# Kernel tuning notes

Hardware: AMD Instinct MI355X
Metric: run time of the kernel (lower is better)

Reference implementation:

```python
import jax, jax.numpy as jnp
import numpy as np

N, E = 20000, 320000
EPS = 1e-5
NEG_SLOPE = 0.2


def gat_conv(x, src, dst, W, att_src, att_dst, bias, num_nodes):
    # W: [Fin, H*C], att_*: [H, C], bias: [H*C]
    H, C = att_src.shape
    h = (x @ W).reshape(num_nodes, H, C)            # [N,H,C]
    a_s = jnp.einsum('nhc,hc->nh', h, att_src)      # [N,H]
    a_d = jnp.einsum('nhc,hc->nh', h, att_dst)      # [N,H]
    e = jax.nn.leaky_relu(a_s[src] + a_d[dst], NEG_SLOPE)  # [E,H]
    m = jax.ops.segment_max(e, dst, num_segments=num_nodes)       # per-dst max (self-loops guarantee non-empty)
    ex = jnp.exp(e - m[dst])
    s = jax.ops.segment_sum(ex, dst, num_segments=num_nodes)
    alpha = ex / s[dst]                              # [E,H] segment softmax
    out = jax.ops.segment_sum(h[src] * alpha[:, :, None], dst, num_segments=num_nodes)  # [N,H,C]
    return out.reshape(num_nodes, H * C) + bias


def batch_norm(x, gamma, beta):
    mu = x.mean(axis=0)
    var = x.var(axis=0)  # biased, as torch BN uses for normalization
    return (x - mu) * jax.lax.rsqrt(var + EPS) * gamma + beta


def setup_inputs() -> dict:
    key = jax.random.key(0)
    ks = jax.random.split(key, 32)
    x = jax.random.normal(ks[0], (N, 512), dtype=jnp.float32)
    edge_index = jax.random.randint(ks[1], (2, E), 0, N, dtype=jnp.int32)
    d = {"x": x, "edge_index": edge_index}
    # layer configs: (Fin, C_out, H)
    cfgs = [(512, 64, 8), (512, 64, 4), (256, 64, 2), (128, 16, 1)]
    i = 2
    for li, (fin, c, h) in enumerate(cfgs, start=1):
        sc = 1.0 / np.sqrt(fin)
        d[f"W{li}"] = jax.random.normal(ks[i], (fin, h * c), dtype=jnp.float32) * sc; i += 1
        d[f"as{li}"] = jax.random.normal(ks[i], (h, c), dtype=jnp.float32) * 0.1; i += 1
        d[f"ad{li}"] = jax.random.normal(ks[i], (h, c), dtype=jnp.float32) * 0.1; i += 1
        d[f"b{li}"] = jnp.zeros((h * c,), dtype=jnp.float32)
        if li < 4:
            d[f"g{li}"] = jnp.ones((h * c,), dtype=jnp.float32)
            d[f"be{li}"] = jnp.zeros((h * c,), dtype=jnp.float32)
    return d


def reference(x, edge_index, W1, as1, ad1, b1, g1, be1, W2, as2, ad2, b2, g2, be2, W3, as3, ad3, b3, g3, be3, W4, as4, ad4, b4):
    num_nodes = x.shape[0]
    loop = jnp.arange(num_nodes, dtype=edge_index.dtype)
    src = jnp.concatenate([edge_index[0], loop])  # add_self_loops=True
    dst = jnp.concatenate([edge_index[1], loop])
    h = gat_conv(x, src, dst, W1, as1, ad1, b1, num_nodes)
    h = jax.nn.elu(batch_norm(h, g1, be1))
    h = gat_conv(h, src, dst, W2, as2, ad2, b2, num_nodes)
    h = jax.nn.elu(batch_norm(h, g2, be2))
    h = gat_conv(h, src, dst, W3, as3, ad3, b3, num_nodes)
    h = jax.nn.elu(batch_norm(h, g3, be3))
    h = gat_conv(h, src, dst, W4, as4, ad4, b4, num_nodes)
    return jax.nn.log_softmax(h, axis=1)
```

## Files before the change

kernel.cpp:

```cpp
#include <hip/hip_runtime.h>
#include <hip/hip_bf16.h>
#include <cstdint>
#include <cstddef>

#define NN 20000
#define EE 320000
#define ET (EE + NN)
#define MPAD 20096
#define SCHUNK 20

typedef __attribute__((ext_vector_type(8))) short  short8;
typedef __attribute__((ext_vector_type(4))) float  floatx4;

__device__ inline unsigned short f2bf(float f) {
    unsigned u = __float_as_uint(f);
    u += 0x7FFFu + ((u >> 16) & 1u);
    return (unsigned short)(u >> 16);
}
__device__ inline float bf2f(unsigned short b) {
    return __uint_as_float(((unsigned)b) << 16);
}
__device__ inline float bflo(unsigned u) { return __uint_as_float(u << 16); }
__device__ inline float bfhi(unsigned u) { return __uint_as_float(u & 0xFFFF0000u); }

__global__ void zero_i32(int* __restrict__ p, int n) {
    int i = blockIdx.x * blockDim.x + threadIdx.x;
    if (i < n) p[i] = 0;
}

__global__ void cvt_a_bf16(const float* __restrict__ in, unsigned short* __restrict__ out,
                           int M, int Mpad, int K) {
    long long base = ((long long)blockIdx.x * blockDim.x + threadIdx.x) * 4;
    if (base >= (long long)Mpad * K) return;
    int row = (int)(base / K);
    float4 v = make_float4(0.f, 0.f, 0.f, 0.f);
    if (row < M) v = *(const float4*)(in + base);
    ushort4 o;
    o.x = f2bf(v.x); o.y = f2bf(v.y); o.z = f2bf(v.z); o.w = f2bf(v.w);
    *(ushort4*)(out + base) = o;
}

#define W1SZ (512 * 512)
#define W2SZ (512 * 256)
#define W3SZ (256 * 128)
__global__ void cvt_w_all(const float* __restrict__ W1, unsigned short* __restrict__ Wt1,
                          const float* __restrict__ W2, unsigned short* __restrict__ Wt2,
                          const float* __restrict__ W3, unsigned short* __restrict__ Wt3) {
    int i = blockIdx.x * blockDim.x + threadIdx.x;
    const float* W; unsigned short* Wt; int K, N, idx;
    if (i < W1SZ)               { W = W1; Wt = Wt1; K = 512; N = 512; idx = i; }
    else if (i < W1SZ + W2SZ)   { W = W2; Wt = Wt2; K = 512; N = 256; idx = i - W1SZ; }
    else if (i < W1SZ + W2SZ + W3SZ) { W = W3; Wt = Wt3; K = 256; N = 128; idx = i - W1SZ - W2SZ; }
    else return;
    int k = idx / N, n = idx - k * N;
    Wt[(size_t)n * K + k] = f2bf(W[idx]);
}

__global__ void count_edges(const int* __restrict__ dst, int* __restrict__ cnt) {
    int e = blockIdx.x * blockDim.x + threadIdx.x;
    if (e >= ET) return;
    int d = (e < EE) ? dst[e] : (e - EE);
    atomicAdd(&cnt[d], 1);
}

__global__ __launch_bounds__(1024) void scan_fast(const int* __restrict__ cnt,
                                                  int* __restrict__ rowp,
                                                  int* __restrict__ wptr, int n) {
    __shared__ int sums[1024];
    const int t = threadIdx.x;
    const int base = t * SCHUNK;
    int local[SCHUNK];
    int acc = 0;
#pragma unroll
    for (int i = 0; i < SCHUNK; ++i) {
        int idx = base + i;
        int v = (idx < n) ? cnt[idx] : 0;
        local[i] = acc;
        acc += v;
    }
    sums[t] = acc;
    __syncthreads();
    for (int o = 1; o < 1024; o <<= 1) {
        int u = (t >= o) ? sums[t - o] : 0;
        __syncthreads();
        sums[t] += u;
        __syncthreads();
    }
    int excl = sums[t] - acc;
#pragma unroll
    for (int i = 0; i < SCHUNK; ++i) {
        int idx = base + i;
        if (idx < n) { int rp = excl + local[i]; rowp[idx] = rp; wptr[idx] = rp; }
    }
    if (t == 1023) rowp[n] = sums[1023];
}

__global__ void fill_edges(const int* __restrict__ src, const int* __restrict__ dst,
                           int* __restrict__ wptr, int* __restrict__ colx) {
    int e = blockIdx.x * blockDim.x + threadIdx.x;
    if (e >= ET) return;
    int s, d;
    if (e < EE) { s = src[e]; d = dst[e]; } else { s = e - EE; d = e - EE; }
    int pos = atomicAdd(&wptr[d], 1);
    colx[pos] = s;
}

__global__ __launch_bounds__(256) void gemm_bf16_fused(
        const unsigned short* __restrict__ A, const unsigned short* __restrict__ Bt,
        unsigned short* __restrict__ hN, float* __restrict__ aS, float* __restrict__ aD,
        const float* __restrict__ atts, const float* __restrict__ attd,
        int M, int N, int K) {
    __shared__ unsigned short As[128][40];
    __shared__ unsigned short Bs[128][40];
    const int t = threadIdx.x;
    const int lane = t & 63, wave = t >> 6;
    const int wm = wave >> 1, wn = wave & 1;
    const int quad = lane >> 4, mrow = lane & 15;
    const int row0 = blockIdx.y * 128, col0 = blockIdx.x * 128;
    const int srow = t >> 2, schunk = (t & 3) * 8;

    floatx4 acc[4][4];
#pragma unroll
    for (int i = 0; i < 4; ++i)
#pragma unroll
        for (int j = 0; j < 4; ++j)
#pragma unroll
            for (int r = 0; r < 4; ++r) acc[i][j][r] = 0.f;

    for (int k0 = 0; k0 < K; k0 += 32) {
        uint4 ra0 = *(const uint4*)(A  + (size_t)(row0 + srow)      * K + k0 + schunk);
        uint4 ra1 = *(const uint4*)(A  + (size_t)(row0 + srow + 64) * K + k0 + schunk);
        uint4 rb0 = *(const uint4*)(Bt + (size_t)(col0 + srow)      * K + k0 + schunk);
        uint4 rb1 = *(const uint4*)(Bt + (size_t)(col0 + srow + 64) * K + k0 + schunk);
        __syncthreads();
        *(uint4*)&As[srow][schunk]      = ra0;
        *(uint4*)&As[srow + 64][schunk] = ra1;
        *(uint4*)&Bs[srow][schunk]      = rb0;
        *(uint4*)&Bs[srow + 64][schunk] = rb1;
        __syncthreads();

        short8 af[4], bfr[4];
#pragma unroll
        for (int i = 0; i < 4; ++i)
            af[i] = *(const short8*)&As[wm * 64 + i * 16 + mrow][quad * 8];
#pragma unroll
        for (int j = 0; j < 4; ++j)
            bfr[j] = *(const short8*)&Bs[wn * 64 + j * 16 + mrow][quad * 8];
#pragma unroll
        for (int i = 0; i < 4; ++i)
#pragma unroll
            for (int j = 0; j < 4; ++j)
                acc[i][j] = __builtin_amdgcn_mfma_f32_16x16x32_bf16(af[i], bfr[j], acc[i][j], 0, 0, 0);
    }

    const int head = (col0 + wn * 64) >> 6;
    float attS[4], attD[4];
#pragma unroll
    for (int j = 0; j < 4; ++j) {
        attS[j] = atts[head * 64 + j * 16 + mrow];
        attD[j] = attd[head * 64 + j * 16 + mrow];
    }

#pragma unroll
    for (int i = 0; i < 4; ++i) {
#pragma unroll
        for (int r = 0; r < 4; ++r) {
            int row = row0 + wm * 64 + i * 16 + quad * 4 + r;
            float ps = acc[i][0][r] * attS[0] + acc[i][1][r] * attS[1]
                     + acc[i][2][r] * attS[2] + acc[i][3][r] * attS[3];
            float pd = acc[i][0][r] * attD[0] + acc[i][1][r] * attD[1]
                     + acc[i][2][r] * attD[2] + acc[i][3][r] * attD[3];
#pragma unroll
            for (int o = 1; o < 16; o <<= 1) {
                ps += __shfl_xor(ps, o);
                pd += __shfl_xor(pd, o);
            }
            if (row < M) {
                if (mrow == 0) {
                    aS[(size_t)head * M + row] = ps;
                    aD[(size_t)head * M + row] = pd;
                }
#pragma unroll
                for (int j = 0; j < 4; ++j)
                    hN[(size_t)row * N + col0 + wn * 64 + j * 16 + mrow] = f2bf(acc[i][j][r]);
            }
        }
    }
}

template <int HH>
__global__ __launch_bounds__(256) void gat_agg_head32(
        const unsigned short* __restrict__ hN,
        const float* __restrict__ aS, const float* __restrict__ aD,
        const int* __restrict__ rowp, const int* __restrict__ colx,
        const float* __restrict__ bias, float* __restrict__ out,
        float* __restrict__ part, int Nn) {
    constexpr int F = HH * 64;
    constexpr int G = 8 / HH;
    __shared__ uint2 pair[4][4][33];
    __shared__ float red[4][16][9];
    const int L = blockIdx.x;
    const int x8 = L & 7;
    const int hd = x8 / G;
    const int nodeblk = (L >> 3) * G + (x8 & (G - 1));
    const int wave = threadIdx.x >> 6, lane = threadIdx.x & 63;
    const int grp = lane >> 4;
    const int q   = lane & 15;
    const int n = nodeblk * 16 + wave * 4 + grp;
    const bool valid = (n < Nn);

    float4 o4 = make_float4(0.f, 0.f, 0.f, 0.f);

    if (valid) {
        const float* aSh = aS + (size_t)hd * Nn;
        const float adv = aD[(size_t)hd * Nn + n];
        const int b0 = rowp[n], b1 = rowp[n + 1];
        const unsigned short* hbase = hN + hd * 64;

        float m, s;
        float a0 = 0.f, a1 = 0.f, a2 = 0.f, a3 = 0.f;

        auto gather = [&](int cnt) {
            const int iters = (cnt + 3) >> 2;
            for (int it = 0; it < iters; ++it) {
                const int j = it << 2;
                uint2 x0 = pair[wave][grp][j + 0];
                uint2 x1 = pair[wave][grp][j + 1];
                uint2 x2 = pair[wave][grp][j + 2];
                uint2 x3 = pair[wave][grp][j + 3];
                uint2 v0 = *(const uint2*)(hbase + (size_t)x0.x * F + q * 4);
                uint2 v1 = *(const uint2*)(hbase + (size_t)x1.x * F + q * 4);
                uint2 v2 = *(const uint2*)(hbase + (size_t)x2.x * F + q * 4);
                uint2 v3 = *(const uint2*)(hbase + (size_t)x3.x * F + q * 4);
                float p0 = __uint_as_float(x0.y), p1 = __uint_as_float(x1.y);
                float p2 = __uint_as_float(x2.y), p3 = __uint_as_float(x3.y);
                a0 += p0 * bflo(v0.x) + p1 * bflo(v1.x) + p2 * bflo(v2.x) + p3 * bflo(v3.x);
                a1 += p0 * bfhi(v0.x) + p1 * bfhi(v1.x) + p2 * bfhi(v2.x) + p3 * bfhi(v3.x);
                a2 += p0 * bflo(v0.y) + p1 * bflo(v1.y) + p2 * bflo(v2.y) + p3 * bflo(v3.y);
                a3 += p0 * bfhi(v0.y) + p1 * bfhi(v1.y) + p2 * bfhi(v2.y) + p3 * bfhi(v3.y);
            }
        };

        {
            const int cnt = min(32, b1 - b0);
            int sn0 = 0, sn1 = 0;
            if (q < cnt)      sn0 = colx[b0 + q];
            if (q + 16 < cnt) sn1 = colx[b0 + q + 16];
            float t0 = aSh[sn0] + adv;
            float t1 = aSh[sn1] + adv;
            float e0 = (q < cnt)      ? ((t0 > 0.f) ? t0 : 0.2f * t0) : -1e30f;
            float e1 = (q + 16 < cnt) ? ((t1 > 0.f) ? t1 : 0.2f * t1) : -1e30f;
            float mc = fmaxf(e0, e1);
#pragma unroll
            for (int o = 8; o > 0; o >>= 1) mc = fmaxf(mc, __shfl_xor(mc, o));
            m = mc;
            float p0 = __expf(e0 - m);
            float p1 = __expf(e1 - m);
            float ps = p0 + p1;
#pragma unroll
            for (int o = 8; o > 0; o >>= 1) ps += __shfl_xor(ps, o);
            s = ps;
            pair[wave][grp][q]      = make_uint2((unsigned)sn0, __float_as_uint(p0));
            pair[wave][grp][q + 16] = make_uint2((unsigned)sn1, __float_as_uint(p1));
            __threadfence_block();
            gather(cnt);
        }

        for (int c0 = b0 + 32; c0 < b1; c0 += 32) {
            __threadfence_block();
            const int cnt = min(32, b1 - c0);
            int sn0 = 0, sn1 = 0;
            if (q < cnt)      sn0 = colx[c0 + q];
            if (q + 16 < cnt) sn1 = colx[c0 + q + 16];
            float t0 = aSh[sn0] + adv;
            float t1 = aSh[sn1] + adv;
            float e0 = (q < cnt)      ? ((t0 > 0.f) ? t0 : 0.2f * t0) : -1e30f;
            float e1 = (q + 16 < cnt) ? ((t1 > 0.f) ? t1 : 0.2f * t1) : -1e30f;
            float mc = fmaxf(e0, e1);
#pragma unroll
            for (int o = 8; o > 0; o >>= 1) mc = fmaxf(mc, __shfl_xor(mc, o));
            float nm = fmaxf(m, mc);
            float sc = __expf(m - nm);
            float p0 = __expf(e0 - nm);
            float p1 = __expf(e1 - nm);
            float ps = p0 + p1;
#pragma unroll
            for (int o = 8; o > 0; o >>= 1) ps += __shfl_xor(ps, o);
            s = s * sc + ps;
            a0 *= sc; a1 *= sc; a2 *= sc; a3 *= sc;
            m = nm;
            pair[wave][grp][q]      = make_uint2((unsigned)sn0, __float_as_uint(p0));
            pair[wave][grp][q + 16] = make_uint2((unsigned)sn1, __float_as_uint(p1));
            __threadfence_block();
            gather(cnt);
        }

        const float inv = 1.f / s;
        const int cb = hd * 64 + q * 4;
        o4.x = a0 * inv + bias[cb + 0];
        o4.y = a1 * inv + bias[cb + 1];
        o4.z = a2 * inv + bias[cb + 2];
        o4.w = a3 * inv + bias[cb + 3];
        *(float4*)(out + (size_t)n * F + cb) = o4;
    }

    float s0 = o4.x, s1 = o4.y, s2 = o4.z, s3 = o4.w;
    float q0 = s0 * s0, q1 = s1 * s1, q2 = s2 * s2, q3 = s3 * s3;
#pragma unroll
    for (int o = 16; o < 64; o <<= 1) {
        s0 += __shfl_xor(s0, o); s1 += __shfl_xor(s1, o);
        s2 += __shfl_xor(s2, o); s3 += __shfl_xor(s3, o);
        q0 += __shfl_xor(q0, o); q1 += __shfl_xor(q1, o);
        q2 += __shfl_xor(q2, o); q3 += __shfl_xor(q3, o);
    }
    if (grp == 0) {
        red[wave][q][0] = s0; red[wave][q][1] = s1;
        red[wave][q][2] = s2; red[wave][q][3] = s3;
        red[wave][q][4] = q0; red[wave][q][5] = q1;
        red[wave][q][6] = q2; red[wave][q][7] = q3;
    }
    __syncthreads();
    if (wave == 0 && lane < 16) {
        float a[8];
#pragma unroll
        for (int k = 0; k < 8; ++k)
            a[k] = red[0][q][k] + red[1][q][k] + red[2][q][k] + red[3][q][k];
        float* pb = part + (size_t)L * 128;
#pragma unroll
        for (int k = 0; k < 4; ++k) {
            pb[q * 4 + k]      = a[k];
            pb[64 + q * 4 + k] = a[4 + k];
        }
    }
}

__global__ __launch_bounds__(256) void gemm_l4_fused(const unsigned short* __restrict__ A,
                                                     const float* __restrict__ B,
                                                     unsigned short* __restrict__ C,
                                                     float* __restrict__ aS, float* __restrict__ aD,
                                                     const float* __restrict__ atts,
                                                     const float* __restrict__ attd,
                                                     int M, int N, int K) {
    __shared__ float As[16][65];
    __shared__ float Bs[16][64];
    const int tid = threadIdx.x;
    const int tx = tid & 15, ty = tid >> 4;
    const int row0 = blockIdx.y * 64, col0 = blockIdx.x * 64;
    const int rA = tid >> 2, kq = (tid & 3) << 2;
    const int rB = tid >> 4, cq = (tid & 15) << 2;
    float acc[4][4] = {};

    for (int k0 = 0; k0 < K; k0 += 16) {
        ushort4 ha = *(const ushort4*)(A + (size_t)(row0 + rA) * K + k0 + kq);
        float4 fb = make_float4(0.f, 0.f, 0.f, 0.f);
        int bcol = col0 + cq;
        if (bcol < N) fb = *(const float4*)(B + (size_t)(k0 + rB) * N + bcol);
        As[kq + 0][rA] = bf2f(ha.x); As[kq + 1][rA] = bf2f(ha.y);
        As[kq + 2][rA] = bf2f(ha.z); As[kq + 3][rA] = bf2f(ha.w);
        *(float4*)&Bs[rB][cq] = fb;
        __syncthreads();
#pragma unroll
        for (int k = 0; k < 16; ++k) {
            float a0 = As[k][ty * 4 + 0];
            float a1 = As[k][ty * 4 + 1];
            float a2 = As[k][ty * 4 + 2];
            float a3 = As[k][ty * 4 + 3];
            float4 b = *(float4*)&Bs[k][tx * 4];
            acc[0][0] += a0 * b.x; acc[0][1] += a0 * b.y; acc[0][2] += a0 * b.z; acc[0][3] += a0 * b.w;
            acc[1][0] += a1 * b.x; acc[1][1] += a1 * b.y; acc[1][2] += a1 * b.z; acc[1][3] += a1 * b.w;
            acc[2][0] += a2 * b.x; acc[2][1] += a2 * b.y; acc[2][2] += a2 * b.z; acc[2][3] += a2 * b.w;
            acc[3][0] += a3 * b.x; acc[3][1] += a3 * b.y; acc[3][2] += a3 * b.z; acc[3][3] += a3 * b.w;
        }
        __syncthreads();
    }
    float as_part[4], ad_part[4];
#pragma unroll
    for (int i = 0; i < 4; ++i) { as_part[i] = 0.f; ad_part[i] = 0.f; }
    if (tx < 4) {
#pragma unroll
        for (int i = 0; i < 4; ++i) {
#pragma unroll
            for (int jj = 0; jj < 4; ++jj) {
                int c = tx * 4 + jj;
                as_part[i] += acc[i][jj] * atts[c];
                ad_part[i] += acc[i][jj] * attd[c];
            }
        }
    }
#pragma unroll
    for (int i = 0; i < 4; ++i) {
        float ps = as_part[i], pd = ad_part[i];
        ps += __shfl_xor(ps, 1); ps += __shfl_xor(ps, 2);
        pd += __shfl_xor(pd, 1); pd += __shfl_xor(pd, 2);
        int r = row0 + ty * 4 + i;
        if (r < M) {
            if (tx == 0) { aS[r] = ps; aD[r] = pd; }
#pragma unroll
            for (int jj = 0; jj < 4; ++jj) {
                int c = col0 + tx * 4 + jj;
                if (c < N) C[(size_t)r * N + c] = f2bf(acc[i][jj]);
            }
        }
    }
}

template <int C>
__global__ void gat_agg_l4_ls(const unsigned short* __restrict__ ht,
                              const float* __restrict__ as, const float* __restrict__ aD,
                              const int* __restrict__ rowp, const int* __restrict__ colx,
                              const float* __restrict__ bias, float* __restrict__ out, int Nn) {
    int n = blockIdx.x * 4 + (threadIdx.x >> 6);
    int lane = threadIdx.x & 63;
    if (n >= Nn) return;
    float adv = aD[n];
    int b0 = rowp[n], b1 = rowp[n + 1];

    float m = -1e30f, s = 0.f, acc = 0.f;
    for (int c0 = b0; c0 < b1; c0 += 64) {
        int cnt = b1 - c0; if (cnt > 64) cnt = 64;
        int sn = 0; float e = -1e30f;
        if (lane < cnt) {
            sn = colx[c0 + lane];
            float tt = as[sn] + adv;
            e = (tt > 0.f) ? tt : 0.2f * tt;
        }
        float mc = e;
#pragma unroll
        for (int o = 32; o > 0; o >>= 1) mc = fmaxf(mc, __shfl_xor(mc, o));
        float nm = fmaxf(m, mc);
        float sc = __expf(m - nm);
        acc *= sc; s *= sc;
        float p = (lane < cnt) ? __expf(e - nm) : 0.f;
        float ps = p;
#pragma unroll
        for (int o = 32; o > 0; o >>= 1) ps += __shfl_xor(ps, o);
        s += ps; m = nm;

        int j = 0;
        for (; j + 4 <= cnt; j += 4) {
            int s0 = __shfl(sn, j),     s1 = __shfl(sn, j + 1);
            int s2 = __shfl(sn, j + 2), s3 = __shfl(sn, j + 3);
            float p0 = __shfl(p, j),     p1 = __shfl(p, j + 1);
            float p2 = __shfl(p, j + 2), p3 = __shfl(p, j + 3);
            float h0 = 0.f, h1 = 0.f, h2 = 0.f, h3 = 0.f;
            if (lane < C) {
                h0 = bf2f(ht[(size_t)s0 * C + lane]);
                h1 = bf2f(ht[(size_t)s1 * C + lane]);
                h2 = bf2f(ht[(size_t)s2 * C + lane]);
                h3 = bf2f(ht[(size_t)s3 * C + lane]);
            }
            acc += p0 * h0 + p1 * h1 + p2 * h2 + p3 * h3;
        }
        for (; j < cnt; ++j) {
            int sj = __shfl(sn, j);
            float pj = __shfl(p, j);
            float hv = (lane < C) ? bf2f(ht[(size_t)sj * C + lane]) : 0.f;
            acc += pj * hv;
        }
    }
    float v = (lane < C) ? (acc / s + bias[lane]) : -1e30f;
    float mx = v;
#pragma unroll
    for (int o = 8; o > 0; o >>= 1) mx = fmaxf(mx, __shfl_xor(mx, o));
    float ex = (lane < C) ? __expf(v - mx) : 0.f;
#pragma unroll
    for (int o = 8; o > 0; o >>= 1) ex += __shfl_xor(ex, o);
    float l = __logf(ex) + mx;
    if (lane < C) out[(size_t)n * C + lane] = v - l;
}

template <int F>
__global__ __launch_bounds__(1024) void bn_reduce_par(const float* __restrict__ part,
                                                      const float* __restrict__ gamma,
                                                      const float* __restrict__ beta,
                                                      float* __restrict__ ss,
                                                      float invN, int NB8) {
    constexpr int G = 512 / F;
    __shared__ float sd[32][33];
    const int t = threadIdx.x;
    const int pr = t >> 5;
    const int tg = t & 31;
    const int c0 = blockIdx.x * 16;
    const int c  = c0 + (tg & 15);
    const int hd = c >> 6;
    const int off = (c & 63) + ((tg < 16) ? 0 : 64);
    float a0 = 0.f, a1 = 0.f, a2 = 0.f, a3 = 0.f;
    for (int g = 0; g < G; ++g) {
        const float* pb = part + (size_t)(hd * G + g) * 128 + off;
        int j = pr;
        for (; j + 96 < NB8; j += 128) {
            a0 += pb[(size_t)(j +  0) * 1024];
            a1 += pb[(size_t)(j + 32) * 1024];
            a2 += pb[(size_t)(j + 64) * 1024];
            a3 += pb[(size_t)(j + 96) * 1024];
        }
        for (; j < NB8; j += 32)
            a0 += pb[(size_t)j * 1024];
    }
    sd[pr][tg] = (a0 + a1) + (a2 + a3);
    __syncthreads();
    if (pr == 0) {
        float tot = sd[0][tg];
#pragma unroll
        for (int r = 1; r < 32; ++r) tot += sd[r][tg];
        sd[0][tg] = tot;
    }
    __syncthreads();
    if (t < 16) {
        int cc = c0 + t;
        float s = sd[0][t];
        float q = sd[0][16 + t];
        float mu = s * invN;
        float var = q * invN - mu * mu;
        float sc = gamma[cc] * rsqrtf(var + 1e-5f);
        ss[cc] = sc;
        ss[F + cc] = beta[cc] - mu * sc;
    }
}

__global__ void bn_apply_elu_bf16(const float* __restrict__ x, const float* __restrict__ ss,
                                  unsigned short* __restrict__ outA,
                                  int Nn, int F, int fmask) {
    long long idx4 = ((long long)blockIdx.x * blockDim.x + threadIdx.x) * 4;
    int row = (int)(idx4 / F);
    ushort4 o = make_ushort4(0, 0, 0, 0);
    if (row < Nn) {
        int c = (int)(idx4 & fmask);
        float4 v = *(const float4*)(x + idx4);
        float v0 = v.x * ss[c + 0] + ss[F + c + 0];
        float v1 = v.y * ss[c + 1] + ss[F + c + 1];
        float v2 = v.z * ss[c + 2] + ss[F + c + 2];
        float v3 = v.w * ss[c + 3] + ss[F + c + 3];
        v0 = (v0 > 0.f) ? v0 : (__expf(v0) - 1.f);
        v1 = (v1 > 0.f) ? v1 : (__expf(v1) - 1.f);
        v2 = (v2 > 0.f) ? v2 : (__expf(v2) - 1.f);
        v3 = (v3 > 0.f) ? v3 : (__expf(v3) - 1.f);
        o.x = f2bf(v0); o.y = f2bf(v1); o.z = f2bf(v2); o.w = f2bf(v3);
    }
    *(ushort4*)(outA + idx4) = o;
}

extern "C" void kernel_launch(void* const* d_in, const int* in_sizes, int n_in,
                              void* d_out, int out_size, void* d_ws, size_t ws_size,
                              hipStream_t stream) {
    const float* x   = (const float*)d_in[0];
    const int*   ei  = (const int*)d_in[1];
    const float* W1  = (const float*)d_in[2];
    const float* as1 = (const float*)d_in[3];
    const float* ad1 = (const float*)d_in[4];
    const float* b1  = (const float*)d_in[5];
    const float* ga1 = (const float*)d_in[6];
    const float* be1 = (const float*)d_in[7];
    const float* W2  = (const float*)d_in[8];
    const float* as2 = (const float*)d_in[9];
    const float* ad2 = (const float*)d_in[10];
    const float* b2  = (const float*)d_in[11];
    const float* ga2 = (const float*)d_in[12];
    const float* be2 = (const float*)d_in[13];
    const float* W3  = (const float*)d_in[14];
    const float* as3 = (const float*)d_in[15];
    const float* ad3 = (const float*)d_in[16];
    const float* b3  = (const float*)d_in[17];
    const float* ga3 = (const float*)d_in[18];
    const float* be3 = (const float*)d_in[19];
    const float* W4  = (const float*)d_in[20];
    const float* as4 = (const float*)d_in[21];
    const float* ad4 = (const float*)d_in[22];
    const float* b4  = (const float*)d_in[23];
    float* outp = (float*)d_out;

    uint8_t* base = (uint8_t*)d_ws;
    size_t off = 0;
    auto alloc = [&](size_t nbytes) -> void* {
        off = (off + 255) & ~(size_t)255;
        void* p = base + off;
        off += nbytes;
        return p;
    };
    float* bufO = (float*)alloc((size_t)NN * 512 * 4);
    unsigned short* bufA = (unsigned short*)alloc((size_t)MPAD * 512 * 2);
    unsigned short* hN   = (unsigned short*)alloc((size_t)NN * 512 * 2);
    unsigned short* Wt1  = (unsigned short*)alloc((size_t)512 * 512 * 2);
    unsigned short* Wt2  = (unsigned short*)alloc((size_t)256 * 512 * 2);
    unsigned short* Wt3  = (unsigned short*)alloc((size_t)128 * 256 * 2);
    float* aSn  = (float*)alloc((size_t)NN * 8 * 4);
    float* aDn  = (float*)alloc((size_t)NN * 8 * 4);
    int*   cnt  = (int*)alloc((size_t)NN * 4);
    int*   rowp = (int*)alloc((size_t)(NN + 1) * 4);
    int*   wptr = (int*)alloc((size_t)NN * 4);
    int*   colx = (int*)alloc((size_t)ET * 4);
    float* bnp  = (float*)alloc((size_t)10048 * 128 * 4);
    float* bns  = (float*)alloc((size_t)1024 * 4);

    const int* srcRow = ei;
    const int* dstRow = ei + EE;

    zero_i32<<<(NN + 255) / 256, 256, 0, stream>>>(cnt, NN);
    count_edges<<<(ET + 255) / 256, 256, 0, stream>>>(dstRow, cnt);
    scan_fast<<<1, 1024, 0, stream>>>(cnt, rowp, wptr, NN);
    fill_edges<<<(ET + 255) / 256, 256, 0, stream>>>(srcRow, dstRow, wptr, colx);

    cvt_w_all<<<(W1SZ + W2SZ + W3SZ) / 256, 256, 0, stream>>>(W1, Wt1, W2, Wt2, W3, Wt3);

    const int NBLK = (NN + 15) / 16;

    {
        cvt_a_bf16<<<((MPAD * 512 / 4) + 255) / 256, 256, 0, stream>>>(x, bufA, NN, MPAD, 512);
        dim3 g(512 / 128, MPAD / 128);
        gemm_bf16_fused<<<g, 256, 0, stream>>>(bufA, Wt1, hN, aSn, aDn, as1, ad1, NN, 512, 512);
        gat_agg_head32<8><<<NBLK * 8, 256, 0, stream>>>(hN, aSn, aDn, rowp, colx, b1, bufO, bnp, NN);
        bn_reduce_par<512><<<512 / 16, 1024, 0, stream>>>(bnp, ga1, be1, bns, 1.0f / NN, NBLK);
        bn_apply_elu_bf16<<<(MPAD * 512 / 4) / 256, 256, 0, stream>>>(bufO, bns, bufA, NN, 512, 511);
    }
    {
        dim3 g(256 / 128, MPAD / 128);
        gemm_bf16_fused<<<g, 256, 0, stream>>>(bufA, Wt2, hN, aSn, aDn, as2, ad2, NN, 256, 512);
        const int nb8 = (NBLK + 1) / 2;
        gat_agg_head32<4><<<nb8 * 8, 256, 0, stream>>>(hN, aSn, aDn, rowp, colx, b2, bufO, bnp, NN);
        bn_reduce_par<256><<<256 / 16, 1024, 0, stream>>>(bnp, ga2, be2, bns, 1.0f / NN, nb8);
        bn_apply_elu_bf16<<<(MPAD * 256 / 4) / 256, 256, 0, stream>>>(bufO, bns, bufA, NN, 256, 255);
    }
    {
        dim3 g(128 / 128, MPAD / 128);
        gemm_bf16_fused<<<g, 256, 0, stream>>>(bufA, Wt3, hN, aSn, aDn, as3, ad3, NN, 128, 256);
        const int nb8 = (NBLK + 3) / 4;
        gat_agg_head32<2><<<nb8 * 8, 256, 0, stream>>>(hN, aSn, aDn, rowp, colx, b3, bufO, bnp, NN);
        bn_reduce_par<128><<<128 / 16, 1024, 0, stream>>>(bnp, ga3, be3, bns, 1.0f / NN, nb8);
        bn_apply_elu_bf16<<<(MPAD * 128 / 4) / 256, 256, 0, stream>>>(bufO, bns, bufA, NN, 128, 127);
    }
    {
        dim3 g(1, (NN + 63) / 64);
        gemm_l4_fused<<<g, 256, 0, stream>>>(bufA, W4, hN, aSn, aDn, as4, ad4, NN, 16, 128);
        gat_agg_l4_ls<16><<<(NN + 3) / 4, 256, 0, stream>>>(hN, aSn, aDn, rowp, colx, b4, outp, NN);
    }
}
```

Baseline: 416.0 us.

## Fuse BatchNorm+ELU into next GEMM's A-load and merge prep conversion kernels

Removes the standalone bn_apply_elu_bf16 kernels. The GEMM of the next layer now reads fp32 aggregation output directly, applies the BN scale and shift plus ELU, and converts to bf16 while staging A tiles. The x conversion and weight conversion kernels are also merged into one prep launch. This saves a full write and re-read of the activation and several launches, but the GEMM now reads twice as many A bytes (fp32) and recomputes exp for each column-block of N.

```diff
diff --git a/kernel.cpp b/kernel.cpp
--- a/kernel.cpp
+++ b/kernel.cpp
@@ -28,32 +28,33 @@
     if (i < n) p[i] = 0;
 }
 
-__global__ void cvt_a_bf16(const float* __restrict__ in, unsigned short* __restrict__ out,
-                           int M, int Mpad, int K) {
-    long long base = ((long long)blockIdx.x * blockDim.x + threadIdx.x) * 4;
-    if (base >= (long long)Mpad * K) return;
-    int row = (int)(base / K);
-    float4 v = make_float4(0.f, 0.f, 0.f, 0.f);
-    if (row < M) v = *(const float4*)(in + base);
-    ushort4 o;
-    o.x = f2bf(v.x); o.y = f2bf(v.y); o.z = f2bf(v.z); o.w = f2bf(v.w);
-    *(ushort4*)(out + base) = o;
-}
-
 #define W1SZ (512 * 512)
 #define W2SZ (512 * 256)
 #define W3SZ (256 * 128)
-__global__ void cvt_w_all(const float* __restrict__ W1, unsigned short* __restrict__ Wt1,
-                          const float* __restrict__ W2, unsigned short* __restrict__ Wt2,
-                          const float* __restrict__ W3, unsigned short* __restrict__ Wt3) {
-    int i = blockIdx.x * blockDim.x + threadIdx.x;
-    const float* W; unsigned short* Wt; int K, N, idx;
-    if (i < W1SZ)               { W = W1; Wt = Wt1; K = 512; N = 512; idx = i; }
-    else if (i < W1SZ + W2SZ)   { W = W2; Wt = Wt2; K = 512; N = 256; idx = i - W1SZ; }
-    else if (i < W1SZ + W2SZ + W3SZ) { W = W3; Wt = Wt3; K = 256; N = 128; idx = i - W1SZ - W2SZ; }
-    else return;
-    int k = idx / N, n = idx - k * N;
-    Wt[(size_t)n * K + k] = f2bf(W[idx]);
+#define NA_BLOCKS (MPAD * 512 / 4 / 256)
+#define NW_BLOCKS ((W1SZ + W2SZ + W3SZ) / 256)
+__global__ void prep_all(const float* __restrict__ x, unsigned short* __restrict__ bufA,
+                         const float* __restrict__ W1, unsigned short* __restrict__ Wt1,
+                         const float* __restrict__ W2, unsigned short* __restrict__ Wt2,
+                         const float* __restrict__ W3, unsigned short* __restrict__ Wt3) {
+    const int b = blockIdx.x;
+    if (b < NA_BLOCKS) {
+        long long base = ((long long)b * 256 + threadIdx.x) * 4;
+        int row = (int)(base / 512);
+        float4 v = make_float4(0.f, 0.f, 0.f, 0.f);
+        if (row < NN) v = *(const float4*)(x + base);
+        ushort4 o;
+        o.x = f2bf(v.x); o.y = f2bf(v.y); o.z = f2bf(v.z); o.w = f2bf(v.w);
+        *(ushort4*)(bufA + base) = o;
+    } else {
+        int i = (b - NA_BLOCKS) * 256 + threadIdx.x;
+        const float* W; unsigned short* Wt; int K, N, idx;
+        if (i < W1SZ)                    { W = W1; Wt = Wt1; K = 512; N = 512; idx = i; }
+        else if (i < W1SZ + W2SZ)        { W = W2; Wt = Wt2; K = 512; N = 256; idx = i - W1SZ; }
+        else                             { W = W3; Wt = Wt3; K = 256; N = 128; idx = i - W1SZ - W2SZ; }
+        int k = idx / N, n = idx - k * N;
+        Wt[(size_t)n * K + k] = f2bf(W[idx]);
+    }
 }
 
 __global__ void count_edges(const int* __restrict__ dst, int* __restrict__ cnt) {
@@ -105,13 +106,17 @@
     colx[pos] = s;
 }
 
+template <bool BN>
 __global__ __launch_bounds__(256) void gemm_bf16_fused(
-        const unsigned short* __restrict__ A, const unsigned short* __restrict__ Bt,
+        const void* __restrict__ Av, const unsigned short* __restrict__ Bt,
         unsigned short* __restrict__ hN, float* __restrict__ aS, float* __restrict__ aD,
         const float* __restrict__ atts, const float* __restrict__ attd,
-        int M, int N, int K) {
+        const float* __restrict__ ssg,
+        int M, int N, int K, int Mreal) {
     __shared__ unsigned short As[128][40];
     __shared__ unsigned short Bs[128][40];
+    __shared__ float ssS[512];
+    __shared__ float ssH[512];
     const int t = threadIdx.x;
     const int lane = t & 63, wave = t >> 6;
     const int wm = wave >> 1, wn = wave & 1;
@@ -119,6 +124,11 @@
     const int row0 = blockIdx.y * 128, col0 = blockIdx.x * 128;
     const int srow = t >> 2, schunk = (t & 3) * 8;
 
+    if (BN) {
+        for (int i = t; i < K; i += 256) { ssS[i] = ssg[i]; ssH[i] = ssg[K + i]; }
+        __syncthreads();
+    }
+
     floatx4 acc[4][4];
 #pragma unroll
     for (int i = 0; i < 4; ++i)
@@ -128,8 +138,39 @@
             for (int r = 0; r < 4; ++r) acc[i][j][r] = 0.f;
 
     for (int k0 = 0; k0 < K; k0 += 32) {
-        uint4 ra0 = *(const uint4*)(A  + (size_t)(row0 + srow)      * K + k0 + schunk);
-        uint4 ra1 = *(const uint4*)(A  + (size_t)(row0 + srow + 64) * K + k0 + schunk);
+        uint4 ra0, ra1;
+        if constexpr (!BN) {
+            const unsigned short* A = (const unsigned short*)Av;
+            ra0 = *(const uint4*)(A + (size_t)(row0 + srow)      * K + k0 + schunk);
+            ra1 = *(const uint4*)(A + (size_t)(row0 + srow + 64) * K + k0 + schunk);
+        } else {
+            const float* A = (const float*)Av;
+            float sc[8], sh[8];
+#pragma unroll
+            for (int i = 0; i < 8; ++i) { sc[i] = ssS[k0 + schunk + i]; sh[i] = ssH[k0 + schunk + i]; }
+            auto stage_row = [&](int arow) -> uint4 {
+                uint4 r = make_uint4(0u, 0u, 0u, 0u);
+                if (arow < Mreal) {
+                    float4 f0 = *(const float4*)(A + (size_t)arow * K + k0 + schunk);
+                    float4 f1 = *(const float4*)(A + (size_t)arow * K + k0 + schunk + 4);
+                    float v[8] = { f0.x, f0.y, f0.z, f0.w, f1.x, f1.y, f1.z, f1.w };
+                    unsigned short h[8];
+#pragma unroll
+                    for (int i = 0; i < 8; ++i) {
+                        float u = v[i] * sc[i] + sh[i];
+                        u = (u > 0.f) ? u : (__expf(u) - 1.f);
+                        h[i] = f2bf(u);
+                    }
+                    r = make_uint4((unsigned)h[0] | ((unsigned)h[1] << 16),
+                                   (unsigned)h[2] | ((unsigned)h[3] << 16),
+                                   (unsigned)h[4] | ((unsigned)h[5] << 16),
+                                   (unsigned)h[6] | ((unsigned)h[7] << 16));
+                }
+                return r;
+            };
+            ra0 = stage_row(row0 + srow);
+            ra1 = stage_row(row0 + srow + 64);
+        }
         uint4 rb0 = *(const uint4*)(Bt + (size_t)(col0 + srow)      * K + k0 + schunk);
         uint4 rb1 = *(const uint4*)(Bt + (size_t)(col0 + srow + 64) * K + k0 + schunk);
         __syncthreads();
@@ -334,13 +375,14 @@
     }
 }
 
-__global__ __launch_bounds__(256) void gemm_l4_fused(const unsigned short* __restrict__ A,
+__global__ __launch_bounds__(256) void gemm_l4_fused(const float* __restrict__ A,
                                                      const float* __restrict__ B,
                                                      unsigned short* __restrict__ C,
                                                      float* __restrict__ aS, float* __restrict__ aD,
                                                      const float* __restrict__ atts,
                                                      const float* __restrict__ attd,
-                                                     int M, int N, int K) {
+                                                     const float* __restrict__ ssg,
+                                                     int M, int N, int K, int Mreal) {
     __shared__ float As[16][65];
     __shared__ float Bs[16][64];
     const int tid = threadIdx.x;
@@ -351,12 +393,25 @@
     float acc[4][4] = {};
 
     for (int k0 = 0; k0 < K; k0 += 16) {
-        ushort4 ha = *(const ushort4*)(A + (size_t)(row0 + rA) * K + k0 + kq);
+        const int arow = row0 + rA;
+        float a0v = 0.f, a1v = 0.f, a2v = 0.f, a3v = 0.f;
+        if (arow < Mreal) {
+            float4 fa = *(const float4*)(A + (size_t)arow * K + k0 + kq);
+            const int c = k0 + kq;
+            a0v = fa.x * ssg[c + 0] + ssg[K + c + 0];
+            a1v = fa.y * ssg[c + 1] + ssg[K + c + 1];
+            a2v = fa.z * ssg[c + 2] + ssg[K + c + 2];
+            a3v = fa.w * ssg[c + 3] + ssg[K + c + 3];
+            a0v = (a0v > 0.f) ? a0v : (__expf(a0v) - 1.f);
+            a1v = (a1v > 0.f) ? a1v : (__expf(a1v) - 1.f);
+            a2v = (a2v > 0.f) ? a2v : (__expf(a2v) - 1.f);
+            a3v = (a3v > 0.f) ? a3v : (__expf(a3v) - 1.f);
+        }
         float4 fb = make_float4(0.f, 0.f, 0.f, 0.f);
         int bcol = col0 + cq;
         if (bcol < N) fb = *(const float4*)(B + (size_t)(k0 + rB) * N + bcol);
-        As[kq + 0][rA] = bf2f(ha.x); As[kq + 1][rA] = bf2f(ha.y);
-        As[kq + 2][rA] = bf2f(ha.z); As[kq + 3][rA] = bf2f(ha.w);
+        As[kq + 0][rA] = a0v; As[kq + 1][rA] = a1v;
+        As[kq + 2][rA] = a2v; As[kq + 3][rA] = a3v;
         *(float4*)&Bs[rB][cq] = fb;
         __syncthreads();
 #pragma unroll
@@ -516,28 +571,6 @@
         ss[cc] = sc;
         ss[F + cc] = beta[cc] - mu * sc;
     }
-}
-
-__global__ void bn_apply_elu_bf16(const float* __restrict__ x, const float* __restrict__ ss,
-                                  unsigned short* __restrict__ outA,
-                                  int Nn, int F, int fmask) {
-    long long idx4 = ((long long)blockIdx.x * blockDim.x + threadIdx.x) * 4;
-    int row = (int)(idx4 / F);
-    ushort4 o = make_ushort4(0, 0, 0, 0);
-    if (row < Nn) {
-        int c = (int)(idx4 & fmask);
-        float4 v = *(const float4*)(x + idx4);
-        float v0 = v.x * ss[c + 0] + ss[F + c + 0];
-        float v1 = v.y * ss[c + 1] + ss[F + c + 1];
-        float v2 = v.z * ss[c + 2] + ss[F + c + 2];
-        float v3 = v.w * ss[c + 3] + ss[F + c + 3];
-        v0 = (v0 > 0.f) ? v0 : (__expf(v0) - 1.f);
-        v1 = (v1 > 0.f) ? v1 : (__expf(v1) - 1.f);
-        v2 = (v2 > 0.f) ? v2 : (__expf(v2) - 1.f);
-        v3 = (v3 > 0.f) ? v3 : (__expf(v3) - 1.f);
-        o.x = f2bf(v0); o.y = f2bf(v1); o.z = f2bf(v2); o.w = f2bf(v3);
-    }
-    *(ushort4*)(outA + idx4) = o;
 }
 
 extern "C" void kernel_launch(void* const* d_in, const int* in_sizes, int n_in,
@@ -600,37 +633,37 @@
     scan_fast<<<1, 1024, 0, stream>>>(cnt, rowp, wptr, NN);
     fill_edges<<<(ET + 255) / 256, 256, 0, stream>>>(srcRow, dstRow, wptr, colx);
 
-    cvt_w_all<<<(W1SZ + W2SZ + W3SZ) / 256, 256, 0, stream>>>(W1, Wt1, W2, Wt2, W3, Wt3);
+    prep_all<<<NA_BLOCKS + NW_BLOCKS, 256, 0, stream>>>(x, bufA, W1, Wt1, W2, Wt2, W3, Wt3);
 
     const int NBLK = (NN + 15) / 16;
 
     {
-        cvt_a_bf16<<<((MPAD * 512 / 4) + 255) / 256, 256, 0, stream>>>(x, bufA, NN, MPAD, 512);
         dim3 g(512 / 128, MPAD / 128);
-        gemm_bf16_fused<<<g, 256, 0, stream>>>(bufA, Wt1, hN, aSn, aDn, as1, ad1, NN, 512, 512);
+        gemm_bf16_fused<false><<<g, 256, 0, stream>>>(bufA, Wt1, hN, aSn, aDn, as1, ad1,
+                                                      nullptr, NN, 512, 512, 0);
         gat_agg_head32<8><<<NBLK * 8, 256, 0, stream>>>(hN, aSn, aDn, rowp, colx, b1, bufO, bnp, NN);
         bn_reduce_par<512><<<512 / 16, 1024, 0, stream>>>(bnp, ga1, be1, bns, 1.0f / NN, NBLK);
-        bn_apply_elu_bf16<<<(MPAD * 512 / 4) / 256, 256, 0, stream>>>(bufO, bns, bufA, NN, 512, 511);
     }
     {
         dim3 g(256 / 128, MPAD / 128);
-        gemm_bf16_fused<<<g, 256, 0, stream>>>(bufA, Wt2, hN, aSn, aDn, as2, ad2, NN, 256, 512);
+        gemm_bf16_fused<true><<<g, 256, 0, stream>>>(bufO, Wt2, hN, aSn, aDn, as2, ad2,
+                                                     bns, NN, 256, 512, NN);
         const int nb8 = (NBLK + 1) / 2;
         gat_agg_head32<4><<<nb8 * 8, 256, 0, stream>>>(hN, aSn, aDn, rowp, colx, b2, bufO, bnp, NN);
         bn_reduce_par<256><<<256 / 16, 1024, 0, stream>>>(bnp, ga2, be2, bns, 1.0f / NN, nb8);
-        bn_apply_elu_bf16<<<(MPAD * 256 / 4) / 256, 256, 0, stream>>>(bufO, bns, bufA, NN, 256, 255);
     }
     {
         dim3 g(128 / 128, MPAD / 128);
-        gemm_bf16_fused<<<g, 256, 0, stream>>>(bufA, Wt3, hN, aSn, aDn, as3, ad3, NN, 128, 256);
+        gemm_bf16_fused<true><<<g, 256, 0, stream>>>(bufO, Wt3, hN, aSn, aDn, as3, ad3,
+                                                     bns, NN, 128, 256, NN);
         const int nb8 = (NBLK + 3) / 4;
         gat_agg_head32<2><<<nb8 * 8, 256, 0, stream>>>(hN, aSn, aDn, rowp, colx, b3, bufO, bnp, NN);
         bn_reduce_par<128><<<128 / 16, 1024, 0, stream>>>(bnp, ga3, be3, bns, 1.0f / NN, nb8);
-        bn_apply_elu_bf16<<<(MPAD * 128 / 4) / 256, 256, 0, stream>>>(bufO, bns, bufA, NN, 128, 127);
     }
     {
         dim3 g(1, (NN + 63) / 64);
-        gemm_l4_fused<<<g, 256, 0, stream>>>(bufA, W4, hN, aSn, aDn, as4, ad4, NN, 16, 128);
+        gemm_l4_fused<<<g, 256, 0, stream>>>(bufO, W4, hN, aSn, aDn, as4, ad4,
+                                             bns, NN, 16, 128, NN);
         gat_agg_l4_ls<16><<<(NN + 3) / 4, 256, 0, stream>>>(hN, aSn, aDn, rowp, colx, b4, outp, NN);
     }
 }
```

Result: no change. 412.1 us (-0.9%).
